# Optimization experiments

Hardware: AMD Instinct MI355X
Metric: run time of the kernel (lower is better)

## Reference

```python
import jax, jax.numpy as jnp
import numpy as np
import math

B, S, D, H = 4, 2048, 1024, 16
HD = D // H  # 64


def setup_inputs() -> dict:
    key = jax.random.key(0)
    ks = jax.random.split(key, 12)
    s_in = 1.0 / math.sqrt(D)
    inp = {
        "x_v": jax.random.normal(ks[0], (B, S, D), jnp.float32),
        "x_k": jax.random.normal(ks[1], (B, S, D), jnp.float32),
        "x_q": jax.random.normal(ks[2], (B, S, D), jnp.float32),
        "mask": jax.random.randint(ks[3], (B, S, S), 0, 2, jnp.int32),
        "Wq": jax.random.normal(ks[4], (H, D, HD), jnp.float32) * s_in,
        "bq": jax.random.normal(ks[5], (H, HD), jnp.float32) * s_in,
        "Wk": jax.random.normal(ks[6], (H, D, HD), jnp.float32) * s_in,
        "bk": jax.random.normal(ks[7], (H, HD), jnp.float32) * s_in,
        "Wv": jax.random.normal(ks[8], (H, D, HD), jnp.float32) * s_in,
        "bv": jax.random.normal(ks[9], (H, HD), jnp.float32) * s_in,
        "Wo": jax.random.normal(ks[10], (D, D), jnp.float32) * s_in,
        "bo": jax.random.normal(ks[11], (D,), jnp.float32) * s_in,
    }
    return inp


def reference(x_v, x_k, x_q, mask, Wq, bq, Wk, bk, Wv, bv, Wo, bo):
    # Batched per-head projections: [B,S,D] x [H,D,E] -> [B,H,S,E]
    q = jnp.einsum("bsd,hde->bhse", x_q, Wq) + bq[None, :, None, :]
    k = jnp.einsum("bsd,hde->bhse", x_k, Wk) + bk[None, :, None, :]
    v = jnp.einsum("bsd,hde->bhse", x_v, Wv) + bv[None, :, None, :]
    scale = 1.0 / math.sqrt(HD)
    scores = jnp.einsum("bhqe,bhke->bhqk", q, k) * scale  # [B,H,Sq,Sk]
    # Faithful to original: masked positions are set to 0 (not -inf) BEFORE softmax
    scores = jnp.where(mask[:, None, :, :] == 0, 0.0, scores)
    attn = jax.nn.softmax(scores, axis=-1)
    z = jnp.einsum("bhqk,bhke->bhqe", attn, v)  # [B,H,Sq,E]
    # Concat over heads in head order (matches torch.cat along dim=2)
    z = z.transpose(0, 2, 1, 3).reshape(B, S, D)
    return z @ Wo + bo
```

## Files before the change

kernel.cpp:

```cpp
#include <hip/hip_runtime.h>

typedef unsigned short u16;
typedef unsigned long long u64;
typedef __attribute__((ext_vector_type(8))) short bf16x8;
typedef __attribute__((ext_vector_type(4))) float f32x4;

#define C_SCALE 0.18033688011112043f

__device__ __forceinline__ u16 f2b(float x) {
  union { float f; unsigned u; } c; c.f = x;
  unsigned r = (c.u + 0x7fffu + ((c.u >> 16) & 1u)) >> 16;
  return (u16)r;
}

__device__ __forceinline__ unsigned pk2(float a, float b) {
#if __has_builtin(__builtin_amdgcn_cvt_pk_bf16_f32)
  typedef __attribute__((ext_vector_type(2))) __bf16 b2;
  b2 r = __builtin_amdgcn_cvt_pk_bf16_f32(a, b);
  union { b2 v; unsigned u; } c; c.v = r;
  return c.u;
#else
  union { float f; unsigned u; } x, y;
  x.f = a; y.f = b;
  return ((x.u + 0x8000u) >> 16) | ((y.u + 0x8000u) & 0xffff0000u);
#endif
}

__device__ __forceinline__ void gll16(const u16* g, u16* l) {
  __builtin_amdgcn_global_load_lds(
      (const __attribute__((address_space(1))) void*)g,
      (__attribute__((address_space(3))) void*)l, 16, 0, 0);
}

__device__ __forceinline__ bf16x8 pblend(f32x4 sa, f32x4 sb, int4 mw) {
  unsigned m0 = (unsigned)mw.x, m1 = (unsigned)mw.y;
  unsigned m2 = (unsigned)mw.z, m3 = (unsigned)mw.w;
  union { unsigned u[4]; bf16x8 v; } pu;
  pu.u[0] = (m0 & pk2(__builtin_amdgcn_exp2f(sa[0]),
                      __builtin_amdgcn_exp2f(sa[1]))) | (~m0 & 0x3f803f80u);
  pu.u[1] = (m1 & pk2(__builtin_amdgcn_exp2f(sa[2]),
                      __builtin_amdgcn_exp2f(sa[3]))) | (~m1 & 0x3f803f80u);
  pu.u[2] = (m2 & pk2(__builtin_amdgcn_exp2f(sb[0]),
                      __builtin_amdgcn_exp2f(sb[1]))) | (~m2 & 0x3f803f80u);
  pu.u[3] = (m3 & pk2(__builtin_amdgcn_exp2f(sb[2]),
                      __builtin_amdgcn_exp2f(sb[3]))) | (~m3 & 0x3f803f80u);
  return pu.v;
}

__global__ __launch_bounds__(256) void cvt_bf16_3(
    const float4* __restrict__ s0, const float4* __restrict__ s1,
    const float4* __restrict__ s2, ushort4* __restrict__ d0,
    ushort4* __restrict__ d1, ushort4* __restrict__ d2, int n4) {
  const int z = blockIdx.y;
  const float4* src = z == 0 ? s0 : z == 1 ? s1 : s2;
  ushort4* dst = z == 0 ? d0 : z == 1 ? d1 : d2;
  int stride = gridDim.x * 256;
  for (int i = blockIdx.x * 256 + threadIdx.x; i < n4; i += stride) {
    float4 v = src[i];
    ushort4 o = { f2b(v.x), f2b(v.y), f2b(v.z), f2b(v.w) };
    dst[i] = o;
  }
}

__global__ __launch_bounds__(256) void transpose_cvt_all(
    const float* __restrict__ Wq, const float* __restrict__ Wk,
    const float* __restrict__ Wv, const float* __restrict__ Wo,
    u16* __restrict__ wq_t, u16* __restrict__ wk_t,
    u16* __restrict__ wv_t, u16* __restrict__ wo_t) {
  __shared__ u16 tile[64][65];
  const int id = blockIdx.x;
  const int which = id >> 8, sub = id & 255;
  const float* s;
  u16* d;
  int R, C, r0, c0;
  if (which < 3) {
    const float* W = which == 0 ? Wq : which == 1 ? Wk : Wv;
    u16* D = which == 0 ? wq_t : which == 1 ? wk_t : wv_t;
    int h = sub >> 4, rt = sub & 15;
    s = W + (size_t)h * 1024 * 64;
    d = D + (size_t)h * 64 * 1024;
    R = 1024; C = 64; r0 = rt * 64; c0 = 0;
  } else {
    s = Wo; d = wo_t;
    R = 1024; C = 1024; r0 = ((sub >> 4) & 15) * 64; c0 = (sub & 15) * 64;
  }
  const int t = threadIdx.x;
#pragma unroll
  for (int rep = 0; rep < 16; ++rep) {
    int idx = rep * 256 + t;
    int i = idx >> 6, j = idx & 63;
    tile[j][i] = f2b(s[(size_t)(r0 + i) * C + c0 + j]);
  }
  __syncthreads();
#pragma unroll
  for (int rep = 0; rep < 16; ++rep) {
    int idx = rep * 256 + t;
    int jj = idx >> 6, ii = idx & 63;
    d[(size_t)(c0 + jj) * R + r0 + ii] = tile[jj][ii];
  }
}

__global__ __launch_bounds__(256) void expand_mask(
    const int4* __restrict__ m, ushort4* __restrict__ mb, int n4) {
  int stride = gridDim.x * 256;
  for (int i = blockIdx.x * 256 + threadIdx.x; i < n4; i += stride) {
    int4 v = m[i];
    ushort4 o = { (u16)(v.x ? 0xFFFF : 0), (u16)(v.y ? 0xFFFF : 0),
                  (u16)(v.z ? 0xFFFF : 0), (u16)(v.w ? 0xFFFF : 0) };
    mb[i] = o;
  }
}

__device__ __forceinline__ void gemm_core(
    const u16* __restrict__ A, const u16* __restrict__ W,
    u16* Asm, u16* Bsm, int s0, int n0, int wv, int lane,
    int m16, int q4, f32x4 acc[4][4]) {
  const int rsub = lane >> 3, csub = lane & 7;
  const int wr = (wv & 1) * 64, wc = (wv >> 1) * 64;
  for (int k0 = 0; k0 < 1024; k0 += 64) {
    __syncthreads();
#pragma unroll
    for (int i = 0; i < 4; ++i) {
      int chunk = wv * 4 + i;
      gll16(A + (size_t)(s0 + chunk * 8 + rsub) * 1024 + k0 + csub * 8,
            Asm + chunk * 512 + lane * 8);
      gll16(W + (size_t)(n0 + chunk * 8 + rsub) * 1024 + k0 + csub * 8,
            Bsm + chunk * 512 + lane * 8);
    }
    __syncthreads();
#pragma unroll
    for (int ks = 0; ks < 2; ++ks) {
      bf16x8 af[4], bfr[4];
#pragma unroll
      for (int i = 0; i < 4; ++i)
        af[i] = *(const bf16x8*)(Asm + (wr + i * 16 + m16) * 64 + ks * 32 + q4 * 8);
#pragma unroll
      for (int j = 0; j < 4; ++j)
        bfr[j] = *(const bf16x8*)(Bsm + (wc + j * 16 + m16) * 64 + ks * 32 + q4 * 8);
#pragma unroll
      for (int i = 0; i < 4; ++i)
#pragma unroll
        for (int j = 0; j < 4; ++j)
          acc[i][j] = __builtin_amdgcn_mfma_f32_16x16x32_bf16(af[i], bfr[j], acc[i][j], 0, 0, 0);
    }
  }
}

__global__ __launch_bounds__(256, 3) void qkv_gemm(
    const u16* __restrict__ xq, const u16* __restrict__ xk,
    const u16* __restrict__ xv, const u16* __restrict__ wq,
    const u16* __restrict__ wk, const u16* __restrict__ wv_,
    const float* __restrict__ bq, const float* __restrict__ bk,
    const float* __restrict__ bv, u16* __restrict__ qb,
    u16* __restrict__ kb, u16* __restrict__ vtb) {
  __shared__ u16 S[17408];
  u16* Asm = S;
  u16* Bsm = S + 8192;
  const int z = blockIdx.z;
  const u16* A = z == 0 ? xq : z == 1 ? xk : xv;
  const u16* W = z == 0 ? wq : z == 1 ? wk : wv_;
  const float* bias = z == 0 ? bq : z == 1 ? bk : bv;
  const int s0 = blockIdx.x * 128, n0 = blockIdx.y * 128;
  const int t = threadIdx.x, wvi = t >> 6, lane = t & 63;
  const int m16 = lane & 15, q4 = lane >> 4;
  const int wr = (wvi & 1) * 64, wc = (wvi >> 1) * 64;
  f32x4 acc[4][4];
#pragma unroll
  for (int i = 0; i < 4; ++i)
#pragma unroll
    for (int j = 0; j < 4; ++j) acc[i][j] = (f32x4){0.f, 0.f, 0.f, 0.f};

  gemm_core(A, W, Asm, Bsm, s0, n0, wvi, lane, m16, q4, acc);

  if (z < 2) {
    u16* out = z == 0 ? qb : kb;
    const float scale = z == 0 ? C_SCALE : 1.0f;
#pragma unroll
    for (int j = 0; j < 4; ++j) {
      int n = n0 + wc + j * 16 + m16;
      int h = n >> 6, e = n & 63;
      float bval = bias[n];
#pragma unroll
      for (int i = 0; i < 4; ++i)
#pragma unroll
        for (int r = 0; r < 4; ++r) {
          int s = s0 + wr + i * 16 + q4 * 4 + r;
          int bi = s >> 11, sl = s & 2047;
          out[((size_t)(bi * 16 + h) * 2048 + sl) * 64 + e] =
              f2b((acc[i][j][r] + bval) * scale);
        }
    }
  } else {
    __syncthreads();
#pragma unroll
    for (int j = 0; j < 4; ++j) {
      int nl = wc + j * 16 + m16;
      float bval = bias[n0 + nl];
#pragma unroll
      for (int i = 0; i < 4; ++i)
#pragma unroll
        for (int r = 0; r < 4; ++r)
          S[nl * 136 + wr + i * 16 + q4 * 4 + r] = f2b(acc[i][j][r] + bval);
    }
    __syncthreads();
    const int bi = s0 >> 11, sl0 = s0 & 2047;
#pragma unroll
    for (int rep = 0; rep < 8; ++rep) {
      int u = rep * 256 + t;
      int rr = u >> 4, cc = (u & 15) * 8;
      int n = n0 + rr, h = n >> 6, e = n & 63;
      *(int4*)(vtb + ((size_t)(bi * 16 + h) * 64 + e) * 2048 + sl0 + cc) =
          *(const int4*)(S + rr * 136 + cc);
    }
  }
}

__global__ __launch_bounds__(256, 2) void out_gemm(
    const u16* __restrict__ Z, const u16* __restrict__ Wot,
    const float* __restrict__ bo, float* __restrict__ out) {
  __shared__ u16 S[17408];
  u16* Asm = S;
  u16* Bsm = S + 8192;
  const int s0 = blockIdx.x * 128, n0 = blockIdx.y * 128;
  const int t = threadIdx.x, wvi = t >> 6, lane = t & 63;
  const int m16 = lane & 15, q4 = lane >> 4;
  const int wr = (wvi & 1) * 64, wc = (wvi >> 1) * 64;
  f32x4 acc[4][4];
#pragma unroll
  for (int i = 0; i < 4; ++i)
#pragma unroll
    for (int j = 0; j < 4; ++j) acc[i][j] = (f32x4){0.f, 0.f, 0.f, 0.f};

  gemm_core(Z, Wot, Asm, Bsm, s0, n0, wvi, lane, m16, q4, acc);

#pragma unroll
  for (int j = 0; j < 4; ++j) {
    int n = n0 + wc + j * 16 + m16;
    float bval = bo[n];
#pragma unroll
    for (int i = 0; i < 4; ++i)
#pragma unroll
      for (int r = 0; r < 4; ++r) {
        int s = s0 + wr + i * 16 + q4 * 4 + r;
        out[(size_t)s * 1024 + n] = acc[i][j][r] + bval;
      }
  }
}

__global__ __launch_bounds__(512, 4) void attn(
    const u16* __restrict__ qb, const u16* __restrict__ kb,
    const u16* __restrict__ vt, const u16* __restrict__ mk,
    u16* __restrict__ zb) {
  __shared__ u16 Kl[2][4096];
  __shared__ u16 Vl[2][4096];
  const int id = blockIdx.x;
  const int qi = id >> 6;
  const int bh = id & 63;
  const int b = bh >> 4, h = bh & 15;
  const int t = threadIdx.x, w = t >> 6, lane = t & 63;
  const int m16 = lane & 15, q4 = lane >> 4;
  const size_t bho = (size_t)bh * 2048;
  const u16* qp = qb + bho * 64;
  const u16* kp = kb + bho * 64;
  const u16* vp = vt + bho * 64;
  const int qbase = qi * 256 + w * 32;

  bf16x8 qa[2][2];
#pragma unroll
  for (int qg = 0; qg < 2; ++qg)
#pragma unroll
    for (int ks = 0; ks < 2; ++ks)
      qa[qg][ks] = *(const bf16x8*)(qp + (size_t)(qbase + qg * 16 + m16) * 64 + ks * 32 + q4 * 8);

  f32x4 oacc[2][4], lacc[2];
#pragma unroll
  for (int qg = 0; qg < 2; ++qg) {
    lacc[qg] = (f32x4){0.f, 0.f, 0.f, 0.f};
#pragma unroll
    for (int g = 0; g < 4; ++g) oacc[qg][g] = (f32x4){0.f, 0.f, 0.f, 0.f};
  }
  bf16x8 ones;
#pragma unroll
  for (int j = 0; j < 8; ++j) ones[j] = (short)0x3f80;

  const u16* mrow[2];
  mrow[0] = mk + ((size_t)b * 2048 + qbase + m16) * 2048;
  mrow[1] = mk + ((size_t)b * 2048 + qbase + 16 + m16) * 2048;

  const int ch = t & 7, rw = t >> 3;
  const int r5 = rw & 31;
  const int sK = (rw & 32) + (((r5 >> 2) & 1) * 16) + (((r5 >> 3) & 3) * 4) + (r5 & 3);

  const int kwc = (ch ^ (sK & 7)) * 8;
  const int vwc = (ch ^ (rw & 7)) * 8;
  const int sw = (m16 & 7) * 8;
  const int rcol0 = (q4 * 8) ^ sw;
  const int rcol1 = (32 + q4 * 8) ^ sw;

  int4 pk0 = *(const int4*)(kp + (size_t)rw * 64 + ch * 8);
  int4 pv0 = *(const int4*)(vp + (size_t)rw * 2048 + ch * 8);
  int4 cm[2][2], nm[2][2];
#pragma unroll
  for (int qg = 0; qg < 2; ++qg)
#pragma unroll
    for (int bb = 0; bb < 2; ++bb)
      cm[qg][bb] = *(const int4*)(mrow[qg] + bb * 32 + q4 * 8);
  *(int4*)(&Kl[0][sK * 64 + kwc]) = pk0;
  *(int4*)(&Vl[0][rw * 64 + vwc]) = pv0;
  __syncthreads();

  for (int kt = 0; kt < 32; ++kt) {
    const int cur = kt & 1;
    if (kt < 31) {
      const int k0n = (kt + 1) * 64;
      pk0 = *(const int4*)(kp + (size_t)(k0n + rw) * 64 + ch * 8);
      pv0 = *(const int4*)(vp + (size_t)rw * 2048 + k0n + ch * 8);
#pragma unroll
      for (int qg = 0; qg < 2; ++qg)
#pragma unroll
        for (int bb = 0; bb < 2; ++bb)
          nm[qg][bb] = *(const int4*)(mrow[qg] + k0n + bb * 32 + q4 * 8);
    }

#pragma unroll
    for (int bb = 0; bb < 2; ++bb) {
      const int rb = bb * 32;
      const int vc = bb ? rcol1 : rcol0;
      bf16x8 kf00 = *(const bf16x8*)(&Kl[cur][(rb + m16) * 64 + rcol0]);
      bf16x8 kf01 = *(const bf16x8*)(&Kl[cur][(rb + m16) * 64 + rcol1]);
      bf16x8 kf10 = *(const bf16x8*)(&Kl[cur][(rb + 16 + m16) * 64 + rcol0]);
      bf16x8 kf11 = *(const bf16x8*)(&Kl[cur][(rb + 16 + m16) * 64 + rcol1]);
      bf16x8 pa[2];
#pragma unroll
      for (int qg = 0; qg < 2; ++qg) {
        f32x4 sa = (f32x4){0.f, 0.f, 0.f, 0.f};
        f32x4 sb = (f32x4){0.f, 0.f, 0.f, 0.f};
        sa = __builtin_amdgcn_mfma_f32_16x16x32_bf16(kf00, qa[qg][0], sa, 0, 0, 0);
        sa = __builtin_amdgcn_mfma_f32_16x16x32_bf16(kf01, qa[qg][1], sa, 0, 0, 0);
        sb = __builtin_amdgcn_mfma_f32_16x16x32_bf16(kf10, qa[qg][0], sb, 0, 0, 0);
        sb = __builtin_amdgcn_mfma_f32_16x16x32_bf16(kf11, qa[qg][1], sb, 0, 0, 0);
        pa[qg] = pblend(sa, sb, cm[qg][bb]);
        lacc[qg] = __builtin_amdgcn_mfma_f32_16x16x32_bf16(pa[qg], ones, lacc[qg], 0, 0, 0);
      }
#pragma unroll
      for (int e = 0; e < 4; ++e) {
        bf16x8 vf = *(const bf16x8*)(&Vl[cur][(e * 16 + m16) * 64 + vc]);
        oacc[0][e] = __builtin_amdgcn_mfma_f32_16x16x32_bf16(pa[0], vf, oacc[0][e], 0, 0, 0);
        oacc[1][e] = __builtin_amdgcn_mfma_f32_16x16x32_bf16(pa[1], vf, oacc[1][e], 0, 0, 0);
      }
    }

    if (kt < 31) {
      const int nxt = cur ^ 1;
      *(int4*)(&Kl[nxt][sK * 64 + kwc]) = pk0;
      *(int4*)(&Vl[nxt][rw * 64 + vwc]) = pv0;
#pragma unroll
      for (int qg = 0; qg < 2; ++qg)
#pragma unroll
        for (int bb = 0; bb < 2; ++bb) cm[qg][bb] = nm[qg][bb];
      __syncthreads();
    }
  }

#pragma unroll
  for (int qg = 0; qg < 2; ++qg) {
#pragma unroll
    for (int r = 0; r < 4; ++r) {
      float inv = __builtin_amdgcn_rcpf(lacc[qg][r]);
      size_t zr = ((size_t)b * 2048 + qbase + qg * 16 + q4 * 4 + r) * 1024 + h * 64;
#pragma unroll
      for (int e = 0; e < 4; ++e) {
        zb[zr + e * 16 + m16] = f2b(oacc[qg][e][r] * inv);
      }
    }
  }
}

extern "C" void kernel_launch(void* const* d_in, const int* in_sizes, int n_in,
                              void* d_out, int out_size, void* d_ws, size_t ws_size,
                              hipStream_t stream) {
  const float* x_v = (const float*)d_in[0];
  const float* x_k = (const float*)d_in[1];
  const float* x_q = (const float*)d_in[2];
  const int* mask = (const int*)d_in[3];
  const float* Wq = (const float*)d_in[4];
  const float* bq = (const float*)d_in[5];
  const float* Wk = (const float*)d_in[6];
  const float* bk = (const float*)d_in[7];
  const float* Wv = (const float*)d_in[8];
  const float* bv = (const float*)d_in[9];
  const float* Wo = (const float*)d_in[10];
  const float* bo = (const float*)d_in[11];
  float* out = (float*)d_out;

  char* ws = (char*)d_ws;
  size_t off = 0;
  auto alloc_u16 = [&](size_t n) {
    u16* p = (u16*)(ws + off);
    off += n * sizeof(u16);
    return p;
  };
  u16* wq_t = alloc_u16((size_t)16 * 64 * 1024);
  u16* wk_t = alloc_u16((size_t)16 * 64 * 1024);
  u16* wv_t = alloc_u16((size_t)16 * 64 * 1024);
  u16* wo_t = alloc_u16((size_t)1024 * 1024);
  u16* qb = alloc_u16((size_t)8192 * 1024);
  u16* kb = alloc_u16((size_t)8192 * 1024);
  u16* vtb = alloc_u16((size_t)8192 * 1024);
  u16* xq16 = alloc_u16((size_t)8192 * 1024);
  u16* xk16 = alloc_u16((size_t)8192 * 1024);
  u16* xv16 = alloc_u16((size_t)8192 * 1024);
  u16* zb = xq16;
  u16* mask16 = xk16;

  transpose_cvt_all<<<dim3(1024), 256, 0, stream>>>(
      Wq, Wk, Wv, Wo, wq_t, wk_t, wv_t, wo_t);
  const int n4 = 8192 * 1024 / 4;
  cvt_bf16_3<<<dim3(512, 3), 256, 0, stream>>>(
      (const float4*)x_q, (const float4*)x_k, (const float4*)x_v,
      (ushort4*)xq16, (ushort4*)xk16, (ushort4*)xv16, n4);
  qkv_gemm<<<dim3(64, 8, 3), 256, 0, stream>>>(
      xq16, xk16, xv16, wq_t, wk_t, wv_t, bq, bk, bv, qb, kb, vtb);
  expand_mask<<<dim3(2048), 256, 0, stream>>>(
      (const int4*)mask, (ushort4*)mask16, 4 * 2048 * 2048 / 4);
  attn<<<dim3(512), 512, 0, stream>>>(qb, kb, vtb, mask16, zb);
  out_gemm<<<dim3(64, 8), 256, 0, stream>>>(zb, wo_t, bo, out);
}
```

Measured before the change: 430.4 us.

## Stage Q/K projection output through LDS and defer mask prefetch

The Q/K projection epilogue now writes tiles into shared memory first and then emits coalesced 16-byte stores in head-major layout, replacing scattered 2-byte global stores. In the attention kernel, the mask loads for the next tile move from the start of the iteration to the end, after compute, and load straight into the live registers. This drops the duplicate nm register set and lowers register pressure. The trade-off is that mask load latency is now exposed just before the barrier instead of being hidden behind the MFMA work.

Result: faster. 391.2 us (-9.1%).

```diff
diff --git a/kernel.cpp b/kernel.cpp
--- a/kernel.cpp
+++ b/kernel.cpp
@@ -175,20 +175,27 @@
   if (z < 2) {
     u16* out = z == 0 ? qb : kb;
     const float scale = z == 0 ? C_SCALE : 1.0f;
+    __syncthreads();
 #pragma unroll
     for (int j = 0; j < 4; ++j) {
-      int n = n0 + wc + j * 16 + m16;
-      int h = n >> 6, e = n & 63;
-      float bval = bias[n];
+      int nl = wc + j * 16 + m16;
+      float bval = bias[n0 + nl];
 #pragma unroll
       for (int i = 0; i < 4; ++i)
 #pragma unroll
-        for (int r = 0; r < 4; ++r) {
-          int s = s0 + wr + i * 16 + q4 * 4 + r;
-          int bi = s >> 11, sl = s & 2047;
-          out[((size_t)(bi * 16 + h) * 2048 + sl) * 64 + e] =
+        for (int r = 0; r < 4; ++r)
+          S[(wr + i * 16 + q4 * 4 + r) * 136 + nl] =
               f2b((acc[i][j][r] + bval) * scale);
-        }
+    }
+    __syncthreads();
+    const int bi = s0 >> 11, sl0 = s0 & 2047;
+#pragma unroll
+    for (int rep = 0; rep < 8; ++rep) {
+      int u = rep * 256 + t;
+      int rr = u >> 4, cc = (u & 15) * 8;
+      int h = (n0 + cc) >> 6, e = cc & 63;
+      *(int4*)(out + ((size_t)(bi * 16 + h) * 2048 + sl0 + rr) * 64 + e) =
+          *(const int4*)(S + rr * 136 + cc);
     }
   } else {
     __syncthreads();
@@ -283,9 +290,8 @@
 #pragma unroll
   for (int j = 0; j < 8; ++j) ones[j] = (short)0x3f80;
 
-  const u16* mrow[2];
-  mrow[0] = mk + ((size_t)b * 2048 + qbase + m16) * 2048;
-  mrow[1] = mk + ((size_t)b * 2048 + qbase + 16 + m16) * 2048;
+  const u16* mrow0 = mk + ((size_t)b * 2048 + qbase + m16) * 2048;
+  const u16* mrow1 = mrow0 + (size_t)16 * 2048;
 
   const int ch = t & 7, rw = t >> 3;
   const int r5 = rw & 31;
@@ -299,12 +305,10 @@
 
   int4 pk0 = *(const int4*)(kp + (size_t)rw * 64 + ch * 8);
   int4 pv0 = *(const int4*)(vp + (size_t)rw * 2048 + ch * 8);
-  int4 cm[2][2], nm[2][2];
-#pragma unroll
-  for (int qg = 0; qg < 2; ++qg)
-#pragma unroll
-    for (int bb = 0; bb < 2; ++bb)
-      cm[qg][bb] = *(const int4*)(mrow[qg] + bb * 32 + q4 * 8);
+  int4 cm00 = *(const int4*)(mrow0 + q4 * 8);
+  int4 cm01 = *(const int4*)(mrow0 + 32 + q4 * 8);
+  int4 cm10 = *(const int4*)(mrow1 + q4 * 8);
+  int4 cm11 = *(const int4*)(mrow1 + 32 + q4 * 8);
   *(int4*)(&Kl[0][sK * 64 + kwc]) = pk0;
   *(int4*)(&Vl[0][rw * 64 + vwc]) = pv0;
   __syncthreads();
@@ -315,11 +319,6 @@
       const int k0n = (kt + 1) * 64;
       pk0 = *(const int4*)(kp + (size_t)(k0n + rw) * 64 + ch * 8);
       pv0 = *(const int4*)(vp + (size_t)rw * 2048 + k0n + ch * 8);
-#pragma unroll
-      for (int qg = 0; qg < 2; ++qg)
-#pragma unroll
-        for (int bb = 0; bb < 2; ++bb)
-          nm[qg][bb] = *(const int4*)(mrow[qg] + k0n + bb * 32 + q4 * 8);
     }
 
 #pragma unroll
@@ -339,7 +338,8 @@
         sa = __builtin_amdgcn_mfma_f32_16x16x32_bf16(kf01, qa[qg][1], sa, 0, 0, 0);
         sb = __builtin_amdgcn_mfma_f32_16x16x32_bf16(kf10, qa[qg][0], sb, 0, 0, 0);
         sb = __builtin_amdgcn_mfma_f32_16x16x32_bf16(kf11, qa[qg][1], sb, 0, 0, 0);
-        pa[qg] = pblend(sa, sb, cm[qg][bb]);
+        const int4 mw = qg == 0 ? (bb ? cm01 : cm00) : (bb ? cm11 : cm10);
+        pa[qg] = pblend(sa, sb, mw);
         lacc[qg] = __builtin_amdgcn_mfma_f32_16x16x32_bf16(pa[qg], ones, lacc[qg], 0, 0, 0);
       }
 #pragma unroll
@@ -352,12 +352,13 @@
 
     if (kt < 31) {
       const int nxt = cur ^ 1;
+      const int k0n = (kt + 1) * 64;
+      cm00 = *(const int4*)(mrow0 + k0n + q4 * 8);
+      cm01 = *(const int4*)(mrow0 + k0n + 32 + q4 * 8);
+      cm10 = *(const int4*)(mrow1 + k0n + q4 * 8);
+      cm11 = *(const int4*)(mrow1 + k0n + 32 + q4 * 8);
       *(int4*)(&Kl[nxt][sK * 64 + kwc]) = pk0;
       *(int4*)(&Vl[nxt][rw * 64 + vwc]) = pv0;
-#pragma unroll
-      for (int qg = 0; qg < 2; ++qg)
-#pragma unroll
-        for (int bb = 0; bb < 2; ++bb) cm[qg][bb] = nm[qg][bb];
       __syncthreads();
     }
   }
```
